# Kernel optimization log

Hardware: AMD Instinct MI355X
Metric: run time of the kernel (lower is better)

Reference implementation:

```python
import jax, jax.numpy as jnp
import numpy as np

DT = 0.005
BETA = 0.9
THR = 0.5
TAU_MIN = 0.02
TAU_STEP = 0.03
TAU_R = 0.002
SLOPE = 25.0  # snntorch fast_sigmoid default surrogate slope

@jax.custom_vjp
def spike_fn(x):
    return (x > 0).astype(x.dtype)

def _spike_fwd(x):
    return spike_fn(x), x

def _spike_bwd(x, g):
    return (g / (SLOPE * jnp.abs(x) + 1.0) ** 2,)

spike_fn.defvjp(_spike_fwd, _spike_bwd)

def setup_inputs() -> dict:
    key = jax.random.key(0)
    ks = jax.random.split(key, 8)
    T, NIN, H, NOUT, P = 1000, 4, 4096, 2, 16
    inv_sqrt_h = 1.0 / np.sqrt(H).astype(np.float32)
    return {
        "x": jax.random.normal(ks[0], (T, NIN + 2, 1), jnp.float32),
        "noise": jax.random.normal(ks[1], (T, H, 1), jnp.float32),
        "Win": jax.random.normal(ks[2], (H, NIN + 2), jnp.float32),
        "Wout": jax.random.normal(ks[3], (NOUT, H), jnp.float32) * inv_sqrt_h,
        "pin": jax.random.normal(ks[4], (H, P), jnp.float32) * inv_sqrt_h,
        "pout": jax.random.normal(ks[5], (H, P), jnp.float32) * inv_sqrt_h,
        "l": jax.random.normal(ks[6], (P,), jnp.float32) * inv_sqrt_h,
        "sigmoid_tau_d": jax.random.normal(ks[7], (H, 1), jnp.float32),
    }

def reference(x, noise, Win, Wout, pin, pout, l, sigmoid_tau_d):
    H = Win.shape[0]
    tau_d = jax.nn.sigmoid(sigmoid_tau_d) * TAU_STEP + TAU_MIN   # [H,1]
    Wr = (l * pin) @ pout.T                                      # [H,H] low-rank recurrent matrix
    decay_r = jnp.exp(jnp.asarray(-DT / TAU_R, x.dtype))         # scalar
    decay_d = jnp.exp(-DT / tau_d)                               # [H,1]
    s_gain = DT / (tau_d * TAU_R)                                # [H,1]

    def step(carry, inp):
        mem, r, s = carry
        xi, ni = inp
        I = Win @ xi + Wr @ r + ni / 10.0                        # [H,1]
        # snntorch Leaky, reset_mechanism='subtract': reset from incoming mem (detached)
        reset = jax.lax.stop_gradient(spike_fn(mem - THR))
        mem = BETA * mem + I - reset * THR
        spk = spike_fn(mem - THR)
        s = s * decay_r + s_gain * spk
        r = decay_d * r + DT * s
        return (mem, r, s), r

    z = jnp.zeros((H, 1), x.dtype)
    _, R = jax.lax.scan(step, (z, z, z), (x, noise))             # R: [T,H,1]
    y = jnp.einsum('oh,thj->toj', Wout, R)                       # [T,O,1]
    return y
```

## Files before the change

### kernel.cpp

```cpp
#include <hip/hip_runtime.h>
#include <math.h>

#define KB       4
#define NTHREADS 256
#define NW       4
#define HID      4096
#define HB       (HID / KB)
#define NPT      4
#define TT       1000
#define PP       16
#define SLOTW    32

#define BETA 0.9f
#define THRV 0.5f
#define DTV  0.005f

template<int CTRL>
__device__ __forceinline__ float dppx(float v) {
    return __int_as_float(__builtin_amdgcn_update_dpp(
        0, __float_as_int(v), CTRL, 0xF, 0xF, true));
}

__device__ __forceinline__ unsigned long long AL(const unsigned long long* p) {
    return __hip_atomic_load(p, __ATOMIC_RELAXED, __HIP_MEMORY_SCOPE_AGENT);
}

__global__ __launch_bounds__(NTHREADS, 1)
void snn_kernel(const float* __restrict__ x,
                const float* __restrict__ noise,
                const float* __restrict__ Win,
                const float* __restrict__ Wout,
                const float* __restrict__ pin,
                const float* __restrict__ pout,
                const float* __restrict__ lvec,
                const float* __restrict__ stdv,
                float* __restrict__ ypart,
                unsigned long long* __restrict__ slots)
{
    const int b    = blockIdx.x;
    const int tid  = threadIdx.x;
    const int wave = tid >> 6;
    const int lane = tid & 63;
    const int h0   = b * HB + tid * NPT;

    const bool lb0 = (lane & 1) != 0;
    const bool lb1 = (lane & 2) != 0;
    const bool lb2 = (lane & 4) != 0;
    const bool lb3 = (lane & 8) != 0;

    const int rbA = (b == 0) ? 1 : 0;
    const int rbB = (b <= 1) ? 2 : 1;
    const int rbC = (b <= 2) ? 3 : 2;

    __shared__ float part[NW][4][16];
    __shared__ float ylds[NW][4][2];
    __shared__ float ubuf[NW][16];

    float lv[PP];
    #pragma unroll
    for (int p = 0; p < PP; p += 4) {
        float4 t4 = *(const float4*)&lvec[p];
        lv[p] = t4.x; lv[p+1] = t4.y; lv[p+2] = t4.z; lv[p+3] = t4.w;
    }
    float pl[NPT][PP], po[NPT][PP];
    #pragma unroll
    for (int j = 0; j < NPT; ++j) {
        #pragma unroll
        for (int p = 0; p < PP; p += 4) {
            float4 a = *(const float4*)&pin[(h0+j)*PP + p];
            pl[j][p]   = a.x*lv[p];   pl[j][p+1] = a.y*lv[p+1];
            pl[j][p+2] = a.z*lv[p+2]; pl[j][p+3] = a.w*lv[p+3];
            float4 e = *(const float4*)&pout[(h0+j)*PP + p];
            po[j][p]   = e.x; po[j][p+1] = e.y;
            po[j][p+2] = e.z; po[j][p+3] = e.w;
        }
    }
    float win[NPT][6];
    #pragma unroll
    for (int j = 0; j < NPT; ++j) {
        const float2* wr = (const float2*)&Win[(h0+j)*6];
        float2 wA = wr[0], wB = wr[1], wC = wr[2];
        win[j][0]=wA.x; win[j][1]=wA.y; win[j][2]=wB.x;
        win[j][3]=wB.y; win[j][4]=wC.x; win[j][5]=wC.y;
    }
    float4 woa = *(const float4*)&Wout[h0];
    float4 wob = *(const float4*)&Wout[HID + h0];

    float4 sd4 = *(const float4*)&stdv[h0];
    float dd[NPT], sg[NPT];
    {
        float sdv[4] = { sd4.x, sd4.y, sd4.z, sd4.w };
        #pragma unroll
        for (int j = 0; j < NPT; ++j) {
            float sig = 1.f / (1.f + expf(-sdv[j]));
            float tau = sig * 0.03f + 0.02f;
            dd[j] = expf(-DTV / tau);
            sg[j] = DTV / (tau * 0.002f);
        }
    }
    const float DECAY_R = expf(-2.5f);

    float mem[NPT], rr[NPT], ss[NPT];
    #pragma unroll
    for (int j = 0; j < NPT; ++j) { mem[j] = 0.f; rr[j] = 0.f; ss[j] = 0.f; }

    const float2* x2 = (const float2*)x;
    float4 nz = *(const float4*)&noise[h0];
    float2 xa = x2[0], xb = x2[1], xc = x2[2];

    float uu[16];
    #pragma unroll
    for (int p = 0; p < 16; ++p) uu[p] = 0.f;

    for (int t = 0; t <= TT; ++t) {
        float4 nz_n = nz; float2 xa_n = xa, xb_n = xb, xc_n = xc;
        if (t < TT - 1) {
            const int tn = t + 1;
            nz_n = *(const float4*)&noise[tn * HID + h0];
            xa_n = x2[tn*3]; xb_n = x2[tn*3+1]; xc_n = x2[tn*3+2];
        }

        float bs = 0.f;
        if (t > 0) {
            const int par = t & 1;
            float pa[18];
            #pragma unroll
            for (int p = 0; p < PP; ++p)
                pa[p] = (po[0][p]*rr[0] + po[1][p]*rr[1])
                      + (po[2][p]*rr[2] + po[3][p]*rr[3]);
            pa[16] = (woa.x*rr[0] + woa.y*rr[1]) + (woa.z*rr[2] + woa.w*rr[3]);
            pa[17] = (wob.x*rr[0] + wob.y*rr[1]) + (wob.z*rr[2] + wob.w*rr[3]);

            float a1[8], yv;
            #pragma unroll
            for (int k = 0; k < 8; ++k) {
                float keep = lb0 ? pa[2*k+1] : pa[2*k];
                float send = lb0 ? pa[2*k]   : pa[2*k+1];
                a1[k] = keep + dppx<0xB1>(send);
            }
            {
                float keep = lb0 ? pa[17] : pa[16];
                float send = lb0 ? pa[16] : pa[17];
                yv = keep + dppx<0xB1>(send);
            }
            float a2[4];
            #pragma unroll
            for (int k = 0; k < 4; ++k) {
                float keep = lb1 ? a1[2*k+1] : a1[2*k];
                float send = lb1 ? a1[2*k]   : a1[2*k+1];
                a2[k] = keep + dppx<0x4E>(send);
            }
            yv += dppx<0x4E>(yv);
            float a3[2];
            #pragma unroll
            for (int k = 0; k < 2; ++k) {
                float keep = lb2 ? a2[2*k+1] : a2[2*k];
                float send = lb2 ? a2[2*k]   : a2[2*k+1];
                a3[k] = keep + __shfl_xor(send, 4, 64);
            }
            yv += __shfl_xor(yv, 4, 64);
            float uvrow;
            {
                float keep = lb3 ? a3[1] : a3[0];
                float send = lb3 ? a3[0] : a3[1];
                uvrow = keep + dppx<0x128>(send);
            }
            yv += dppx<0x128>(yv);

            part[wave][lane >> 4][lane & 15] = uvrow;
            if ((lane & 15) < 2) ylds[wave][lane >> 4][lane & 1] = yv;
            __syncthreads();

            float ybs = 0.f;
            if (lane < 16) {
                float t0 = (part[0][0][lane] + part[0][1][lane])
                         + (part[0][2][lane] + part[0][3][lane]);
                float t1 = (part[1][0][lane] + part[1][1][lane])
                         + (part[1][2][lane] + part[1][3][lane]);
                float t2 = (part[2][0][lane] + part[2][1][lane])
                         + (part[2][2][lane] + part[2][3][lane]);
                float t3 = (part[3][0][lane] + part[3][1][lane])
                         + (part[3][2][lane] + part[3][3][lane]);
                bs = (t0 + t1) + (t2 + t3);
            } else if (lane < 18) {
                const int yi = lane - 16;
                float t0 = (ylds[0][0][yi] + ylds[0][1][yi])
                         + (ylds[0][2][yi] + ylds[0][3][yi]);
                float t1 = (ylds[1][0][yi] + ylds[1][1][yi])
                         + (ylds[1][2][yi] + ylds[1][3][yi]);
                float t2 = (ylds[2][0][yi] + ylds[2][1][yi])
                         + (ylds[2][2][yi] + ylds[2][3][yi]);
                float t3 = (ylds[3][0][yi] + ylds[3][1][yi])
                         + (ylds[3][2][yi] + ylds[3][3][yi]);
                ybs = (t0 + t1) + (t2 + t3);
            }

            if (wave == 0) {
                if (lane < 16 && t < TT) {
                    union { float f; unsigned u; } cv; cv.f = bs;
                    unsigned long long pk = ((unsigned long long)(unsigned)t << 32)
                                          | (unsigned long long)cv.u;
                    __hip_atomic_store(&slots[(size_t)(par*KB + b)*SLOTW + lane], pk,
                                       __ATOMIC_RELAXED, __HIP_MEMORY_SCOPE_AGENT);
                } else if (lane >= 16 && lane < 18) {
                    ypart[(size_t)b * (2*TT) + (t-1)*2 + (lane-16)] = ybs;
                }
            }
        }

        if (t < TT) {
            float nzv[4] = { nz.x, nz.y, nz.z, nz.w };
            float pre[NPT];
            #pragma unroll
            for (int j = 0; j < NPT; ++j) {
                float xw = win[j][0]*xa.x + win[j][1]*xa.y
                         + win[j][2]*xb.x + win[j][3]*xb.y
                         + win[j][4]*xc.x + win[j][5]*xc.y;
                float rst = (mem[j] - THRV > 0.f) ? THRV : 0.f;
                pre[j] = BETA*mem[j] + xw + nzv[j] / 10.0f - rst;
            }

            if (t > 0) {
                const int par = t & 1;
                const size_t sb = (size_t)par * KB;
                {
                    const unsigned long long* t0p = &slots[(sb + rbA)*SLOTW + 15];
                    const unsigned long long* t1p = &slots[(sb + rbB)*SLOTW + 15];
                    const unsigned long long* t2p = &slots[(sb + rbC)*SLOTW + 15];
                    unsigned long long w0, w1, w2;
                    int sp = 0;
                    do {
                        w0 = AL(t0p); w1 = AL(t1p); w2 = AL(t2p);
                    } while ((((unsigned)(w0 >> 32) != (unsigned)t) |
                              ((unsigned)(w1 >> 32) != (unsigned)t) |
                              ((unsigned)(w2 >> 32) != (unsigned)t)) &&
                             ++sp < (1 << 20));
                }
                float f0 = 0.f, f1 = 0.f, f2 = 0.f;
                int ok = 1;
                if (lane < 16) {
                    const unsigned long long* pa_ = &slots[(sb + rbA)*SLOTW + lane];
                    const unsigned long long* pb_ = &slots[(sb + rbB)*SLOTW + lane];
                    const unsigned long long* pc_ = &slots[(sb + rbC)*SLOTW + lane];
                    unsigned long long va, vb, vc;
                    int sp2 = 0;
                    do {
                        va = AL(pa_); vb = AL(pb_); vc = AL(pc_);
                        ok = ((unsigned)(va >> 32) == (unsigned)t)
                           & ((unsigned)(vb >> 32) == (unsigned)t)
                           & ((unsigned)(vc >> 32) == (unsigned)t);
                    } while (!__all(ok) && ++sp2 < (1 << 18));
                    union { unsigned u; float f; } c0, c1, c2;
                    c0.u = (unsigned)va; c1.u = (unsigned)vb; c2.u = (unsigned)vc;
                    f0 = c0.f; f1 = c1.f; f2 = c2.f;
                }
                float total = (b < 2) ? ((bs + f0) + (f1 + f2))
                                      : ((f0 + f1) + (f2 + bs));
                if (lane < 16) ubuf[wave][lane] = total;
                float4 u0 = *(const float4*)&ubuf[wave][0];
                float4 u1 = *(const float4*)&ubuf[wave][4];
                float4 u2 = *(const float4*)&ubuf[wave][8];
                float4 u3 = *(const float4*)&ubuf[wave][12];
                uu[0]=u0.x; uu[1]=u0.y; uu[2]=u0.z; uu[3]=u0.w;
                uu[4]=u1.x; uu[5]=u1.y; uu[6]=u1.z; uu[7]=u1.w;
                uu[8]=u2.x; uu[9]=u2.y; uu[10]=u2.z; uu[11]=u2.w;
                uu[12]=u3.x; uu[13]=u3.y; uu[14]=u3.z; uu[15]=u3.w;
            }

            #pragma unroll
            for (int j = 0; j < NPT; ++j) {
                float ra = pl[j][0]*uu[0];
                float rb2_ = pl[j][8]*uu[8];
                #pragma unroll
                for (int p = 1; p < 8; ++p) {
                    ra   += pl[j][p]*uu[p];
                    rb2_ += pl[j][p+8]*uu[p+8];
                }
                float rec = ra + rb2_;
                mem[j] = pre[j] + rec;
                float spk = (mem[j] - THRV > 0.f) ? 1.f : 0.f;
                ss[j] = ss[j]*DECAY_R + sg[j]*spk;
                rr[j] = dd[j]*rr[j] + DTV*ss[j];
            }
            nz = nz_n; xa = xa_n; xb = xb_n; xc = xc_n;
        }
    }
}

__global__ void ysum_kernel(const float* __restrict__ yp, float* __restrict__ out) {
    int i = blockIdx.x * blockDim.x + threadIdx.x;
    if (i < 2 * TT) {
        float a = yp[i];
        float b = yp[2*TT + i];
        float c = yp[2*2*TT + i];
        float d = yp[3*2*TT + i];
        out[i] = (a + b) + (c + d);
    }
}

extern "C" void kernel_launch(void* const* d_in, const int* in_sizes, int n_in,
                              void* d_out, int out_size, void* d_ws, size_t ws_size,
                              hipStream_t stream)
{
    const float* x     = (const float*)d_in[0];
    const float* noise = (const float*)d_in[1];
    const float* Win   = (const float*)d_in[2];
    const float* Wout  = (const float*)d_in[3];
    const float* pin   = (const float*)d_in[4];
    const float* pout  = (const float*)d_in[5];
    const float* l     = (const float*)d_in[6];
    const float* stdv  = (const float*)d_in[7];
    float* out = (float*)d_out;
    unsigned long long* slots = (unsigned long long*)d_ws;
    float* ypart = (float*)((char*)d_ws + 4096);

    hipLaunchKernelGGL(snn_kernel, dim3(KB), dim3(NTHREADS), 0, stream,
                       x, noise, Win, Wout, pin, pout, l, stdv,
                       ypart, slots);
    hipLaunchKernelGGL(ysum_kernel, dim3((2*TT + 255)/256), dim3(256), 0, stream,
                       ypart, out);
}
```

Measured before the change: 1.897 ms.

## Precompute spike-independent projections before cross-block wait to shorten critical path

Splits the r/s update into a linear part that does not depend on the current spike and a spike correction. The linear projection onto pout and Wout is computed before waiting on other blocks' slots, so only a small correction sits on the post-wait critical path. The in-wave reduction now finishes with xor shuffles across 16/32 lanes, which shrinks the shared-memory partials and the cross-wave sum. The slot polling drops the separate lane-15 tag spin, and next-step loads move after the exchange. The extra registers for linear partials may add pressure, and reordering the floating-point sums can change rounding.

```diff
diff --git a/kernel.cpp b/kernel.cpp
--- a/kernel.cpp
+++ b/kernel.cpp
@@ -23,6 +23,9 @@
 
 __device__ __forceinline__ unsigned long long AL(const unsigned long long* p) {
     return __hip_atomic_load(p, __ATOMIC_RELAXED, __HIP_MEMORY_SCOPE_AGENT);
+}
+__device__ __forceinline__ void AS(unsigned long long* p, unsigned long long v) {
+    __hip_atomic_store(p, v, __ATOMIC_RELAXED, __HIP_MEMORY_SCOPE_AGENT);
 }
 
 __global__ __launch_bounds__(NTHREADS, 1)
@@ -52,8 +55,7 @@
     const int rbB = (b <= 1) ? 2 : 1;
     const int rbC = (b <= 2) ? 3 : 2;
 
-    __shared__ float part[NW][4][16];
-    __shared__ float ylds[NW][4][2];
+    __shared__ float part[NW][20];
     __shared__ float ubuf[NW][16];
 
     float lv[PP];
@@ -70,9 +72,9 @@
             float4 a = *(const float4*)&pin[(h0+j)*PP + p];
             pl[j][p]   = a.x*lv[p];   pl[j][p+1] = a.y*lv[p+1];
             pl[j][p+2] = a.z*lv[p+2]; pl[j][p+3] = a.w*lv[p+3];
-            float4 e = *(const float4*)&pout[(h0+j)*PP + p];
-            po[j][p]   = e.x; po[j][p+1] = e.y;
-            po[j][p+2] = e.z; po[j][p+3] = e.w;
+            float4 e4 = *(const float4*)&pout[(h0+j)*PP + p];
+            po[j][p]   = e4.x; po[j][p+1] = e4.y;
+            po[j][p+2] = e4.z; po[j][p+3] = e4.w;
         }
     }
     float win[NPT][6];
@@ -99,10 +101,15 @@
         }
     }
     const float DECAY_R = expf(-2.5f);
+    const float DTE     = DTV * DECAY_R;
 
     float mem[NPT], rr[NPT], ss[NPT];
-    #pragma unroll
-    for (int j = 0; j < NPT; ++j) { mem[j] = 0.f; rr[j] = 0.f; ss[j] = 0.f; }
+    float pre[NPT], rlin[NPT], slin[NPT];
+    float palin[PP], yalin = 0.f, yblin = 0.f;
+    #pragma unroll
+    for (int j = 0; j < NPT; ++j) { mem[j]=0.f; rr[j]=0.f; ss[j]=0.f; }
+    #pragma unroll
+    for (int p = 0; p < PP; ++p) palin[p] = 0.f;
 
     const float2* x2 = (const float2*)x;
     float4 nz = *(const float4*)&noise[h0];
@@ -113,176 +120,155 @@
     for (int p = 0; p < 16; ++p) uu[p] = 0.f;
 
     for (int t = 0; t <= TT; ++t) {
-        float4 nz_n = nz; float2 xa_n = xa, xb_n = xb, xc_n = xc;
-        if (t < TT - 1) {
-            const int tn = t + 1;
-            nz_n = *(const float4*)&noise[tn * HID + h0];
-            xa_n = x2[tn*3]; xb_n = x2[tn*3+1]; xc_n = x2[tn*3+2];
-        }
+        const int par = t & 1;
 
         float bs = 0.f;
         if (t > 0) {
-            const int par = t & 1;
-            float pa[18];
-            #pragma unroll
-            for (int p = 0; p < PP; ++p)
-                pa[p] = (po[0][p]*rr[0] + po[1][p]*rr[1])
-                      + (po[2][p]*rr[2] + po[3][p]*rr[3]);
-            pa[16] = (woa.x*rr[0] + woa.y*rr[1]) + (woa.z*rr[2] + woa.w*rr[3]);
-            pa[17] = (wob.x*rr[0] + wob.y*rr[1]) + (wob.z*rr[2] + wob.w*rr[3]);
-
-            float a1[8], yv;
-            #pragma unroll
-            for (int k = 0; k < 8; ++k) {
-                float keep = lb0 ? pa[2*k+1] : pa[2*k];
-                float send = lb0 ? pa[2*k]   : pa[2*k+1];
-                a1[k] = keep + dppx<0xB1>(send);
-            }
-            {
-                float keep = lb0 ? pa[17] : pa[16];
-                float send = lb0 ? pa[16] : pa[17];
-                yv = keep + dppx<0xB1>(send);
-            }
-            float a2[4];
-            #pragma unroll
-            for (int k = 0; k < 4; ++k) {
-                float keep = lb1 ? a1[2*k+1] : a1[2*k];
-                float send = lb1 ? a1[2*k]   : a1[2*k+1];
-                a2[k] = keep + dppx<0x4E>(send);
-            }
-            yv += dppx<0x4E>(yv);
-            float a3[2];
-            #pragma unroll
-            for (int k = 0; k < 2; ++k) {
-                float keep = lb2 ? a2[2*k+1] : a2[2*k];
-                float send = lb2 ? a2[2*k]   : a2[2*k+1];
-                a3[k] = keep + __shfl_xor(send, 4, 64);
-            }
-            yv += __shfl_xor(yv, 4, 64);
-            float uvrow;
-            {
-                float keep = lb3 ? a3[1] : a3[0];
-                float send = lb3 ? a3[0] : a3[1];
-                uvrow = keep + dppx<0x128>(send);
-            }
-            yv += dppx<0x128>(yv);
-
-            part[wave][lane >> 4][lane & 15] = uvrow;
-            if ((lane & 15) < 2) ylds[wave][lane >> 4][lane & 1] = yv;
-            __syncthreads();
-
-            float ybs = 0.f;
-            if (lane < 16) {
-                float t0 = (part[0][0][lane] + part[0][1][lane])
-                         + (part[0][2][lane] + part[0][3][lane]);
-                float t1 = (part[1][0][lane] + part[1][1][lane])
-                         + (part[1][2][lane] + part[1][3][lane]);
-                float t2 = (part[2][0][lane] + part[2][1][lane])
-                         + (part[2][2][lane] + part[2][3][lane]);
-                float t3 = (part[3][0][lane] + part[3][1][lane])
-                         + (part[3][2][lane] + part[3][3][lane]);
-                bs = (t0 + t1) + (t2 + t3);
-            } else if (lane < 18) {
-                const int yi = lane - 16;
-                float t0 = (ylds[0][0][yi] + ylds[0][1][yi])
-                         + (ylds[0][2][yi] + ylds[0][3][yi]);
-                float t1 = (ylds[1][0][yi] + ylds[1][1][yi])
-                         + (ylds[1][2][yi] + ylds[1][3][yi]);
-                float t2 = (ylds[2][0][yi] + ylds[2][1][yi])
-                         + (ylds[2][2][yi] + ylds[2][3][yi]);
-                float t3 = (ylds[3][0][yi] + ylds[3][1][yi])
-                         + (ylds[3][2][yi] + ylds[3][3][yi]);
-                ybs = (t0 + t1) + (t2 + t3);
-            }
-
+            if (lane < 18) {
+                bs = (part[0][lane] + part[1][lane])
+                   + (part[2][lane] + part[3][lane]);
+            }
             if (wave == 0) {
-                if (lane < 16 && t < TT) {
-                    union { float f; unsigned u; } cv; cv.f = bs;
-                    unsigned long long pk = ((unsigned long long)(unsigned)t << 32)
-                                          | (unsigned long long)cv.u;
-                    __hip_atomic_store(&slots[(size_t)(par*KB + b)*SLOTW + lane], pk,
-                                       __ATOMIC_RELAXED, __HIP_MEMORY_SCOPE_AGENT);
-                } else if (lane >= 16 && lane < 18) {
-                    ypart[(size_t)b * (2*TT) + (t-1)*2 + (lane-16)] = ybs;
+                if (lane < 16) {
+                    if (t < TT) {
+                        union { float f; unsigned u; } cv; cv.f = bs;
+                        unsigned long long pk =
+                            ((unsigned long long)(unsigned)t << 32)
+                          | (unsigned long long)cv.u;
+                        AS(&slots[(size_t)(par*KB + b)*SLOTW + lane], pk);
+                    }
+                } else if (lane < 18) {
+                    ypart[(size_t)b*(2*TT) + (t-1)*2 + (lane-16)] = bs;
                 }
             }
         }
 
         if (t < TT) {
             float nzv[4] = { nz.x, nz.y, nz.z, nz.w };
-            float pre[NPT];
             #pragma unroll
             for (int j = 0; j < NPT; ++j) {
                 float xw = win[j][0]*xa.x + win[j][1]*xa.y
                          + win[j][2]*xb.x + win[j][3]*xb.y
                          + win[j][4]*xc.x + win[j][5]*xc.y;
                 float rst = (mem[j] - THRV > 0.f) ? THRV : 0.f;
-                pre[j] = BETA*mem[j] + xw + nzv[j] / 10.0f - rst;
-            }
-
-            if (t > 0) {
-                const int par = t & 1;
-                const size_t sb = (size_t)par * KB;
-                {
-                    const unsigned long long* t0p = &slots[(sb + rbA)*SLOTW + 15];
-                    const unsigned long long* t1p = &slots[(sb + rbB)*SLOTW + 15];
-                    const unsigned long long* t2p = &slots[(sb + rbC)*SLOTW + 15];
-                    unsigned long long w0, w1, w2;
-                    int sp = 0;
-                    do {
-                        w0 = AL(t0p); w1 = AL(t1p); w2 = AL(t2p);
-                    } while ((((unsigned)(w0 >> 32) != (unsigned)t) |
-                              ((unsigned)(w1 >> 32) != (unsigned)t) |
-                              ((unsigned)(w2 >> 32) != (unsigned)t)) &&
-                             ++sp < (1 << 20));
-                }
-                float f0 = 0.f, f1 = 0.f, f2 = 0.f;
-                int ok = 1;
-                if (lane < 16) {
-                    const unsigned long long* pa_ = &slots[(sb + rbA)*SLOTW + lane];
-                    const unsigned long long* pb_ = &slots[(sb + rbB)*SLOTW + lane];
-                    const unsigned long long* pc_ = &slots[(sb + rbC)*SLOTW + lane];
-                    unsigned long long va, vb, vc;
-                    int sp2 = 0;
-                    do {
-                        va = AL(pa_); vb = AL(pb_); vc = AL(pc_);
-                        ok = ((unsigned)(va >> 32) == (unsigned)t)
-                           & ((unsigned)(vb >> 32) == (unsigned)t)
-                           & ((unsigned)(vc >> 32) == (unsigned)t);
-                    } while (!__all(ok) && ++sp2 < (1 << 18));
-                    union { unsigned u; float f; } c0, c1, c2;
-                    c0.u = (unsigned)va; c1.u = (unsigned)vb; c2.u = (unsigned)vc;
-                    f0 = c0.f; f1 = c1.f; f2 = c2.f;
-                }
-                float total = (b < 2) ? ((bs + f0) + (f1 + f2))
-                                      : ((f0 + f1) + (f2 + bs));
-                if (lane < 16) ubuf[wave][lane] = total;
-                float4 u0 = *(const float4*)&ubuf[wave][0];
-                float4 u1 = *(const float4*)&ubuf[wave][4];
-                float4 u2 = *(const float4*)&ubuf[wave][8];
-                float4 u3 = *(const float4*)&ubuf[wave][12];
-                uu[0]=u0.x; uu[1]=u0.y; uu[2]=u0.z; uu[3]=u0.w;
-                uu[4]=u1.x; uu[5]=u1.y; uu[6]=u1.z; uu[7]=u1.w;
-                uu[8]=u2.x; uu[9]=u2.y; uu[10]=u2.z; uu[11]=u2.w;
-                uu[12]=u3.x; uu[13]=u3.y; uu[14]=u3.z; uu[15]=u3.w;
-            }
-
+                pre[j]  = BETA*mem[j] + xw + nzv[j] / 10.0f - rst;
+                rlin[j] = dd[j]*rr[j] + DTE*ss[j];
+                slin[j] = DECAY_R*ss[j];
+            }
+            #pragma unroll
+            for (int p = 0; p < PP; ++p)
+                palin[p] = (po[0][p]*rlin[0] + po[1][p]*rlin[1])
+                         + (po[2][p]*rlin[2] + po[3][p]*rlin[3]);
+            yalin = (woa.x*rlin[0]+woa.y*rlin[1]) + (woa.z*rlin[2]+woa.w*rlin[3]);
+            yblin = (wob.x*rlin[0]+wob.y*rlin[1]) + (wob.z*rlin[2]+wob.w*rlin[3]);
+        }
+
+        if (t > 0 && t < TT) {
+            const size_t sb = (size_t)par * KB;
+            float f0 = 0.f, f1 = 0.f, f2 = 0.f;
+            if (lane < 16) {
+                const unsigned long long* pa_ = &slots[(sb + rbA)*SLOTW + lane];
+                const unsigned long long* pb_ = &slots[(sb + rbB)*SLOTW + lane];
+                const unsigned long long* pc_ = &slots[(sb + rbC)*SLOTW + lane];
+                unsigned long long va, vb, vc;
+                int sp = 0;
+                do {
+                    va = AL(pa_); vb = AL(pb_); vc = AL(pc_);
+                } while ((((unsigned)(va >> 32) != (unsigned)t) |
+                          ((unsigned)(vb >> 32) != (unsigned)t) |
+                          ((unsigned)(vc >> 32) != (unsigned)t)) &&
+                         ++sp < (1 << 20));
+                union { unsigned u; float f; } c0, c1, c2;
+                c0.u = (unsigned)va; c1.u = (unsigned)vb; c2.u = (unsigned)vc;
+                f0 = c0.f; f1 = c1.f; f2 = c2.f;
+            }
+            float total = (b < 2) ? ((bs + f0) + (f1 + f2))
+                                  : ((f0 + f1) + (f2 + bs));
+            if (lane < 16) ubuf[wave][lane] = total;
+            float4 u0 = *(const float4*)&ubuf[wave][0];
+            float4 u1 = *(const float4*)&ubuf[wave][4];
+            float4 u2 = *(const float4*)&ubuf[wave][8];
+            float4 u3 = *(const float4*)&ubuf[wave][12];
+            uu[0]=u0.x; uu[1]=u0.y; uu[2]=u0.z; uu[3]=u0.w;
+            uu[4]=u1.x; uu[5]=u1.y; uu[6]=u1.z; uu[7]=u1.w;
+            uu[8]=u2.x; uu[9]=u2.y; uu[10]=u2.z; uu[11]=u2.w;
+            uu[12]=u3.x; uu[13]=u3.y; uu[14]=u3.z; uu[15]=u3.w;
+        }
+
+        if (t < TT) {
+            if (t < TT - 1) {
+                const int tn = t + 1;
+                nz = *(const float4*)&noise[tn * HID + h0];
+                xa = x2[tn*3]; xb = x2[tn*3+1]; xc = x2[tn*3+2];
+            }
+
+            float rs[NPT];
             #pragma unroll
             for (int j = 0; j < NPT; ++j) {
-                float ra = pl[j][0]*uu[0];
-                float rb2_ = pl[j][8]*uu[8];
+                float ra  = pl[j][0]*uu[0];
+                float rb_ = pl[j][8]*uu[8];
                 #pragma unroll
                 for (int p = 1; p < 8; ++p) {
-                    ra   += pl[j][p]*uu[p];
-                    rb2_ += pl[j][p+8]*uu[p+8];
+                    ra  += pl[j][p]*uu[p];
+                    rb_ += pl[j][p+8]*uu[p+8];
                 }
-                float rec = ra + rb2_;
-                mem[j] = pre[j] + rec;
-                float spk = (mem[j] - THRV > 0.f) ? 1.f : 0.f;
-                ss[j] = ss[j]*DECAY_R + sg[j]*spk;
-                rr[j] = dd[j]*rr[j] + DTV*ss[j];
-            }
-            nz = nz_n; xa = xa_n; xb = xb_n; xc = xc_n;
+                mem[j] = pre[j] + (ra + rb_);
+                bool spk = (mem[j] - THRV > 0.f);
+                float rspk = spk ? DTV*sg[j] : 0.f;
+                ss[j] = slin[j] + (spk ? sg[j] : 0.f);
+                rr[j] = rlin[j] + rspk;
+                rs[j] = rspk;
+            }
+            float pa[18];
+            #pragma unroll
+            for (int p = 0; p < PP; ++p)
+                pa[p] = palin[p] + ((po[0][p]*rs[0] + po[1][p]*rs[1])
+                                 +  (po[2][p]*rs[2] + po[3][p]*rs[3]));
+            pa[16] = yalin + ((woa.x*rs[0]+woa.y*rs[1]) + (woa.z*rs[2]+woa.w*rs[3]));
+            pa[17] = yblin + ((wob.x*rs[0]+wob.y*rs[1]) + (wob.z*rs[2]+wob.w*rs[3]));
+
+            float a1[8], yv;
+            #pragma unroll
+            for (int k = 0; k < 8; ++k) {
+                float keep = lb0 ? pa[2*k+1] : pa[2*k];
+                float send = lb0 ? pa[2*k]   : pa[2*k+1];
+                a1[k] = keep + dppx<0xB1>(send);
+            }
+            {
+                float keep = lb0 ? pa[17] : pa[16];
+                float send = lb0 ? pa[16] : pa[17];
+                yv = keep + dppx<0xB1>(send);
+            }
+            float a2[4];
+            #pragma unroll
+            for (int k = 0; k < 4; ++k) {
+                float keep = lb1 ? a1[2*k+1] : a1[2*k];
+                float send = lb1 ? a1[2*k]   : a1[2*k+1];
+                a2[k] = keep + dppx<0x4E>(send);
+            }
+            yv += dppx<0x4E>(yv);
+            float a3[2];
+            #pragma unroll
+            for (int k = 0; k < 2; ++k) {
+                float keep = lb2 ? a2[2*k+1] : a2[2*k];
+                float send = lb2 ? a2[2*k]   : a2[2*k+1];
+                a3[k] = keep + __shfl_xor(send, 4, 64);
+            }
+            yv += __shfl_xor(yv, 4, 64);
+            float uv;
+            {
+                float keep = lb3 ? a3[1] : a3[0];
+                float send = lb3 ? a3[0] : a3[1];
+                uv = keep + dppx<0x128>(send);
+            }
+            yv += dppx<0x128>(yv);
+            uv += __shfl_xor(uv, 16, 64);
+            uv += __shfl_xor(uv, 32, 64);
+            yv += __shfl_xor(yv, 16, 64);
+            yv += __shfl_xor(yv, 32, 64);
+
+            if (lane < 18) part[wave][lane] = (lane < 16) ? uv : yv;
+            __syncthreads();
         }
     }
 }
```

Result: faster. 1.611 ms (median of 2 runs) (-15.1%).
